# Optimization experiments

Hardware: AMD Instinct MI355X
Metric: run time of the kernel (lower is better)

The kernel has to match this reference:

```python
import jax, jax.numpy as jnp
import numpy as np

D = 64          # d_model
H = 128         # ffn_hidden_dim
N = 10000       # nodes
E = 50000       # edges
NEG_SLOPE = 0.01  # LeakyReLU default


def setup_inputs() -> dict:
    key = jax.random.key(0)
    ks = jax.random.split(key, 10)
    x = jax.random.normal(ks[0], (N, D), dtype=jnp.float32)
    edge_index = jax.random.randint(ks[1], (2, E), 0, N)
    edge_attr = jax.random.normal(ks[2], (E, D), dtype=jnp.float32)
    # MapE2NxN params (stored as [in, out] so forward is x @ W + b)
    w1 = jax.random.normal(ks[3], (D, H), dtype=jnp.float32) / np.sqrt(D)
    b1 = jnp.zeros((H,), dtype=jnp.float32)
    w2 = jax.random.normal(ks[4], (H, D * D), dtype=jnp.float32) / np.sqrt(H)
    b2 = jnp.zeros((D * D,), dtype=jnp.float32)
    # NNConv root weight + bias
    root = jax.random.normal(ks[5], (D, D), dtype=jnp.float32) / np.sqrt(D)
    bias = jnp.zeros((D,), dtype=jnp.float32)
    # LayerNorm affine params
    gamma = jnp.ones((D,), dtype=jnp.float32)
    beta = jnp.zeros((D,), dtype=jnp.float32)
    return {"x": x, "edge_attr": edge_attr, "gamma": gamma, "beta": beta,
            "w1": w1, "b1": b1, "w2": w2, "b2": b2,
            "root": root, "bias": bias, "edge_index": edge_index}


def _layer_norm(h, gamma, beta, eps=1e-5):
    mu = jnp.mean(h, axis=-1, keepdims=True)
    var = jnp.var(h, axis=-1, keepdims=True)
    return (h - mu) * jax.lax.rsqrt(var + eps) * gamma + beta


def _leaky_relu(h):
    return jnp.where(h >= 0, h, NEG_SLOPE * h)


def reference(x, edge_attr, gamma, beta, w1, b1, w2, b2, root, bias, edge_index):
    src, dst = edge_index[0], edge_index[1]
    # DeepGCNLayer block='res+': pre-activation norm -> act -> (dropout p=0) -> conv -> residual
    h = _leaky_relu(_layer_norm(x, gamma, beta))
    # MapE2NxN on edge attributes -> per-edge [D, D] weight matrix
    we = _leaky_relu(edge_attr @ w1 + b1) @ w2 + b2   # [E, D*D]
    we = we.reshape(E, D, D)
    # per-edge matvec with source node features (PyG NNConv message)
    msg = jnp.einsum('ed,edf->ef', h[src], we)        # [E, D]
    # scatter-mean aggregate into destination nodes
    agg = jax.ops.segment_sum(msg, dst, num_segments=N)
    cnt = jax.ops.segment_sum(jnp.ones((E,), dtype=msg.dtype), dst, num_segments=N)
    agg = agg / jnp.maximum(cnt, 1.0)[:, None]
    # root transform + bias, then residual
    out = agg + h @ root + bias
    return x + out
```

## Files before the change

### kernel.cpp

```cpp
#include <hip/hip_runtime.h>

#define NS 10000
#define DD 64
#define HH 128
#define EE 50000
#define SLOPE 0.01f

typedef __attribute__((ext_vector_type(8))) short short8;
typedef __attribute__((ext_vector_type(4))) float f32x4;

static __device__ __forceinline__ unsigned short f2bf(float f) {
  unsigned int u = __float_as_uint(f);
  u += 0x7fff + ((u >> 16) & 1);
  return (unsigned short)(u >> 16);
}

__device__ __forceinline__ float wave_sum64(float v) {
  #pragma unroll
  for (int m = 32; m >= 1; m >>= 1) v += __shfl_xor(v, m, 64);
  return v;
}

__global__ __launch_bounds__(256) void k_tw2z(const float* __restrict__ w2,
    unsigned short* __restrict__ w2t2, float4* __restrict__ zbase, int zn4) {
  __shared__ float tile[64][65];
  int t = threadIdx.x;
  int k = blockIdx.x;
  for (int off = k * 256 + t; off < zn4; off += 128 * 256)
    zbase[off] = make_float4(0.f, 0.f, 0.f, 0.f);
  #pragma unroll
  for (int i = 0; i < 16; ++i) {
    int idx = t + i * 256;
    tile[idx >> 6][idx & 63] = w2[k * (DD * DD) + idx];
  }
  __syncthreads();
  #pragma unroll
  for (int it = 0; it < 2; ++it) {
    int slot = t + it * 256;
    int f = slot >> 3, l8 = slot & 7;
    short8 o;
    #pragma unroll
    for (int j = 0; j < 8; ++j) o[j] = f2bf(tile[l8 * 8 + j][f]);
    *(short8*)(w2t2 + ((size_t)(f * HH + k)) * DD + l8 * 8) = o;
  }
}

__global__ __launch_bounds__(256) void k_prep(const float* __restrict__ x,
    const float* __restrict__ gamma, const float* __restrict__ beta,
    float* __restrict__ h, unsigned short* __restrict__ hbf,
    const float* __restrict__ ea, unsigned short* __restrict__ eabf,
    const float* __restrict__ w1, unsigned short* __restrict__ w1t,
    const float* __restrict__ b2, unsigned short* __restrict__ b2t,
    const int* __restrict__ ei, int* __restrict__ cntsrc,
    int* __restrict__ cntdst) {
  int gid = blockIdx.x * 256 + threadIdx.x;
  if (gid < EE) {
    atomicAdd(&cntsrc[ei[gid]], 1);
    atomicAdd(&cntdst[ei[EE + gid]], 1);
  }
  if (gid < EE * DD / 8) {
    const float4* sp = (const float4*)(ea + (size_t)gid * 8);
    float4 v0 = sp[0], v1 = sp[1];
    short8 o;
    o[0] = f2bf(v0.x); o[1] = f2bf(v0.y); o[2] = f2bf(v0.z); o[3] = f2bf(v0.w);
    o[4] = f2bf(v1.x); o[5] = f2bf(v1.y); o[6] = f2bf(v1.z); o[7] = f2bf(v1.w);
    *(short8*)(eabf + (size_t)gid * 8) = o;
  }
  if (gid < DD * HH) {
    int d = gid & 63, hc = gid >> 6;
    w1t[gid] = f2bf(w1[d * HH + hc]);
  }
  if (gid < DD * DD) {
    int d = gid & 63, f = gid >> 6;
    b2t[gid] = f2bf(b2[d * DD + f]);
  }
  int wid = threadIdx.x >> 6;
  int lane = threadIdx.x & 63;
  int row = blockIdx.x * 4 + wid;
  if (row >= NS) return;
  float v = x[row * DD + lane];
  float s = wave_sum64(v);
  float s2 = wave_sum64(v * v);
  float mu = s * (1.0f / 64.0f);
  float var = s2 * (1.0f / 64.0f) - mu * mu;
  float r = rsqrtf(var + 1e-5f);
  float hn = (v - mu) * r * gamma[lane] + beta[lane];
  float hv = hn >= 0.f ? hn : SLOPE * hn;
  h[row * DD + lane] = hv;
  hbf[row * DD + lane] = f2bf(hv);
}

__global__ __launch_bounds__(1024) void k_scan(const int* __restrict__ cntsrc,
    int* __restrict__ rowptr, int* __restrict__ cursor) {
  __shared__ int ps[1024];
  int t = threadIdx.x;
  const int CH = (NS + 1023) / 1024;
  int base = t * CH;
  int sum = 0;
  for (int i = 0; i < CH; ++i) {
    int idx = base + i;
    if (idx < NS) sum += cntsrc[idx];
  }
  ps[t] = sum;
  __syncthreads();
  for (int off = 1; off < 1024; off <<= 1) {
    int v = (t >= off) ? ps[t - off] : 0;
    __syncthreads();
    ps[t] += v;
    __syncthreads();
  }
  int run = ps[t] - sum;
  for (int i = 0; i < CH; ++i) {
    int idx = base + i;
    if (idx < NS) {
      rowptr[idx] = run;
      cursor[idx] = run;
      run += cntsrc[idx];
    }
  }
  if (t == 1023) rowptr[NS] = run;
}

#define UBLK 782
#define CBLK 157
__global__ __launch_bounds__(256) void k_mid(
    const unsigned short* __restrict__ eabf, const unsigned short* __restrict__ w1t,
    const float* __restrict__ b1, unsigned short* __restrict__ ubf,
    const unsigned short* __restrict__ hbf, const unsigned short* __restrict__ b2t,
    float* __restrict__ cc, const int* __restrict__ ei,
    int* __restrict__ cursor, int* __restrict__ eord) {
  int t = threadIdx.x;
  int bid = blockIdx.x;
  int gid = bid * 256 + t;
  if (gid < EE) {
    int s = ei[gid];
    int pos = atomicAdd(&cursor[s], 1);
    eord[pos] = gid;
  }
  int w = t >> 6, lane = t & 63, lr = lane & 15, lg = lane >> 4;
  if (bid < UBLK) {
    int r0 = bid * 64 + w * 16;
    int ra = r0 + lr; if (ra >= EE) ra = EE - 1;
    short8 a0 = *(const short8*)(eabf + (size_t)ra * DD + lg * 8);
    short8 a1 = *(const short8*)(eabf + (size_t)ra * DD + 32 + lg * 8);
    short8 bb0[8], bb1[8];
    #pragma unroll
    for (int ni = 0; ni < 8; ++ni) {
      const unsigned short* bp = w1t + (ni * 16 + lr) * DD;
      bb0[ni] = *(const short8*)(bp + lg * 8);
      bb1[ni] = *(const short8*)(bp + 32 + lg * 8);
    }
    f32x4 acc[8] = {};
    #pragma unroll
    for (int ni = 0; ni < 8; ++ni) {
      acc[ni] = __builtin_amdgcn_mfma_f32_16x16x32_bf16(a0, bb0[ni], acc[ni], 0, 0, 0);
      acc[ni] = __builtin_amdgcn_mfma_f32_16x16x32_bf16(a1, bb1[ni], acc[ni], 0, 0, 0);
    }
    #pragma unroll
    for (int ni = 0; ni < 8; ++ni) {
      int col = ni * 16 + lr;
      float bb = b1[col];
      #pragma unroll
      for (int reg = 0; reg < 4; ++reg) {
        int gr = r0 + lg * 4 + reg;
        if (gr < EE) {
          float vv = acc[ni][reg] + bb;
          ubf[(size_t)gr * HH + col] = f2bf(vv >= 0.f ? vv : SLOPE * vv);
        }
      }
    }
  } else if (bid < UBLK + CBLK) {
    int row0 = (bid - UBLK) * 64;
    short8 a[4][2];
    #pragma unroll
    for (int mi = 0; mi < 4; ++mi) {
      int ra = row0 + mi * 16 + lr; if (ra >= NS) ra = NS - 1;
      a[mi][0] = *(const short8*)(hbf + (size_t)ra * DD + lg * 8);
      a[mi][1] = *(const short8*)(hbf + (size_t)ra * DD + 32 + lg * 8);
    }
    const unsigned short* bp = b2t + (w * 16 + lr) * DD;
    short8 b0 = *(const short8*)(bp + lg * 8);
    short8 b1v = *(const short8*)(bp + 32 + lg * 8);
    f32x4 acc[4] = {};
    #pragma unroll
    for (int mi = 0; mi < 4; ++mi) {
      acc[mi] = __builtin_amdgcn_mfma_f32_16x16x32_bf16(a[mi][0], b0, acc[mi], 0, 0, 0);
      acc[mi] = __builtin_amdgcn_mfma_f32_16x16x32_bf16(a[mi][1], b1v, acc[mi], 0, 0, 0);
    }
    #pragma unroll
    for (int mi = 0; mi < 4; ++mi)
      #pragma unroll
      for (int reg = 0; reg < 4; ++reg) {
        int gr = row0 + mi * 16 + lg * 4 + reg;
        if (gr < NS) cc[(size_t)gr * DD + w * 16 + lr] = acc[mi][reg];
      }
  }
}

__global__ __launch_bounds__(256) void k_T_mfma(
    const unsigned short* __restrict__ hbf, const unsigned short* __restrict__ w2t2,
    unsigned short* __restrict__ T, int n0, int n1) {
  __shared__ unsigned short As[64][72];
  __shared__ unsigned short Bs[256 * 72];
  int t = threadIdx.x;
  int row0 = n0 + blockIdx.x * 64;
  if (row0 >= n1) return;
  int col0 = blockIdx.y * 256;
  #pragma unroll
  for (int i = 0; i < 2; ++i) {
    int idx = t + i * 256;
    int r = idx >> 3, cc = (idx & 7) * 8;
    int gr = row0 + r;
    short8 v = {};
    if (gr < n1) v = *(const short8*)(hbf + (size_t)gr * DD + cc);
    *(short8*)(&As[r][cc]) = v;
  }
  #pragma unroll
  for (int i = 0; i < 8; ++i) {
    int idx = t + i * 256;
    int cL = idx >> 3, rr = (idx & 7) * 8;
    int gc = col0 + cL;
    short8 v = *(const short8*)(w2t2 + (size_t)gc * DD + rr);
    *(short8*)(&Bs[cL * 72 + rr]) = v;
  }
  __syncthreads();
  int w = t >> 6, lane = t & 63;
  int lr = lane & 15, lg = lane >> 4;
  f32x4 acc[4][4] = {};
  #pragma unroll
  for (int kk = 0; kk < 64; kk += 32) {
    short8 a[4], b[4];
    #pragma unroll
    for (int mi = 0; mi < 4; ++mi)
      a[mi] = *(const short8*)(&As[mi * 16 + lr][kk + lg * 8]);
    #pragma unroll
    for (int ni = 0; ni < 4; ++ni)
      b[ni] = *(const short8*)(&Bs[(w * 64 + ni * 16 + lr) * 72 + kk + lg * 8]);
    #pragma unroll
    for (int mi = 0; mi < 4; ++mi)
      #pragma unroll
      for (int ni = 0; ni < 4; ++ni)
        acc[mi][ni] = __builtin_amdgcn_mfma_f32_16x16x32_bf16(
            a[mi], b[ni], acc[mi][ni], 0, 0, 0);
  }
  __syncthreads();
  #pragma unroll
  for (int mi = 0; mi < 4; ++mi)
    #pragma unroll
    for (int ni = 0; ni < 4; ++ni) {
      int col = w * 64 + ni * 16 + lr;
      #pragma unroll
      for (int reg = 0; reg < 4; ++reg)
        Bs[(mi * 16 + lg * 4 + reg) * 268 + col] = f2bf(acc[mi][ni][reg]);
    }
  __syncthreads();
  #pragma unroll
  for (int i = 0; i < 8; ++i) {
    int idx = t + i * 256;
    int row = idx >> 5, seg = idx & 31;
    int gr = row0 + row;
    if (gr < n1) {
      short8 v = *(const short8*)(&Bs[row * 268 + seg * 8]);
      *(short8*)(T + (size_t)(gr - n0) * (HH * DD) + col0 + seg * 8) = v;
    }
  }
}

__global__ __launch_bounds__(256) void k_msg_wave(
    const unsigned short* __restrict__ ubf, const unsigned short* __restrict__ T,
    const float* __restrict__ cc, const int* __restrict__ ei,
    const int* __restrict__ rowptr, const int* __restrict__ eord,
    float* __restrict__ agg, int n0, int n1) {
  int wid = threadIdx.x >> 6;
  int lane = threadIdx.x & 63;
  int s = n0 + blockIdx.x * 64 + blockIdx.y * 4 + wid;
  if (s >= n1) return;
  int beg = rowptr[s];
  int deg = rowptr[s + 1] - beg;
  if (deg == 0) return;
  int lr = lane & 15, lg = lane >> 4;
  int ev = 0, dv = 0;
  if (lane < 16 && lane < deg) {
    ev = eord[beg + lane];
    dv = ei[EE + ev];
  }
  const unsigned short* tp = T + (size_t)(s - n0) * (HH * DD);
  short8 b[4][4];
  #pragma unroll
  for (int ft = 0; ft < 4; ++ft)
    #pragma unroll
    for (int kk = 0; kk < 4; ++kk)
      b[ft][kk] =
          *(const short8*)(tp + (ft * 16 + lr) * HH + kk * 32 + lg * 8);
  float clv[4];
  #pragma unroll
  for (int ft = 0; ft < 4; ++ft) clv[ft] = cc[(size_t)s * DD + ft * 16 + lr];

  for (int p0 = 0; p0 < deg; p0 += 16) {
    if (p0) {
      ev = 0; dv = 0;
      if (lane < 16 && p0 + lane < deg) {
        ev = eord[beg + p0 + lane];
        dv = ei[EE + ev];
      }
    }
    int el = __shfl(ev, (p0 + lr < deg) ? lr : 0);
    const unsigned short* up = ubf + (size_t)el * HH;
    short8 au[4];
    #pragma unroll
    for (int kk = 0; kk < 4; ++kk)
      au[kk] = *(const short8*)(up + kk * 32 + lg * 8);
    f32x4 acc[4] = {};
    #pragma unroll
    for (int kk = 0; kk < 4; ++kk)
      #pragma unroll
      for (int ft = 0; ft < 4; ++ft)
        acc[ft] = __builtin_amdgcn_mfma_f32_16x16x32_bf16(au[kk], b[ft][kk],
                                                          acc[ft], 0, 0, 0);
    #pragma unroll
    for (int reg = 0; reg < 4; ++reg) {
      int eidx = p0 + lg * 4 + reg;
      int dstn = __shfl(dv, lg * 4 + reg);
      if (eidx < deg) {
        #pragma unroll
        for (int ft = 0; ft < 4; ++ft)
          atomicAdd(&agg[(size_t)dstn * DD + ft * 16 + lr],
                    acc[ft][reg] + clv[ft]);
      }
    }
  }
}

__global__ __launch_bounds__(256) void k_final(const float* __restrict__ x,
    const float* __restrict__ h, const float* __restrict__ root,
    const float* __restrict__ bias, const float* __restrict__ agg,
    const int* __restrict__ cnt, float* __restrict__ out) {
  __shared__ float Bs[DD][DD + 1];
  __shared__ float As[32][DD];
  int t = threadIdx.x;
  #pragma unroll
  for (int i = 0; i < 16; ++i) {
    int idx = t + i * 256;
    Bs[idx >> 6][idx & 63] = root[idx];
  }
  int row0 = blockIdx.x * 32;
  #pragma unroll
  for (int i = 0; i < 8; ++i) {
    int idx = t + i * 256;
    int r = idx >> 6, d = idx & 63;
    int gr = row0 + r;
    As[r][d] = (gr < NS) ? h[gr * DD + d] : 0.f;
  }
  __syncthreads();
  int r = t >> 3;
  int c0 = (t & 7) * 8;
  int gr = row0 + r;
  if (gr >= NS) return;
  float acc[8] = {};
  for (int d = 0; d < DD; ++d) {
    float a = As[r][d];
    #pragma unroll
    for (int j = 0; j < 8; ++j) acc[j] += a * Bs[d][c0 + j];
  }
  float inv = 1.0f / fmaxf((float)cnt[gr], 1.0f);
  #pragma unroll
  for (int j = 0; j < 8; ++j) {
    size_t gi = (size_t)gr * DD + c0 + j;
    out[gi] = x[gi] + agg[gi] * inv + acc[j] + bias[c0 + j];
  }
}

extern "C" void kernel_launch(void* const* d_in, const int* in_sizes, int n_in,
                              void* d_out, int out_size, void* d_ws, size_t ws_size,
                              hipStream_t stream) {
  const float* x     = (const float*)d_in[0];
  const float* ea    = (const float*)d_in[1];
  const float* gamma = (const float*)d_in[2];
  const float* beta  = (const float*)d_in[3];
  const float* w1    = (const float*)d_in[4];
  const float* b1    = (const float*)d_in[5];
  const float* w2    = (const float*)d_in[6];
  const float* b2    = (const float*)d_in[7];
  const float* root  = (const float*)d_in[8];
  const float* bias  = (const float*)d_in[9];
  const int*   ei    = (const int*)d_in[10];
  float* out = (float*)d_out;

  char* p = (char*)d_ws;
  auto carve = [&](size_t bytes) {
    char* q = p;
    p += (bytes + 255) & ~(size_t)255;
    return q;
  };
  float* h             = (float*)carve(sizeof(float) * NS * DD);
  unsigned short* hbf  = (unsigned short*)carve(sizeof(short) * NS * DD);
  float* cc            = (float*)carve(sizeof(float) * NS * DD);
  unsigned short* w2t2 = (unsigned short*)carve(sizeof(short) * HH * DD * DD);
  unsigned short* w1t  = (unsigned short*)carve(sizeof(short) * DD * HH);
  unsigned short* b2t  = (unsigned short*)carve(sizeof(short) * DD * DD);
  unsigned short* eabf = (unsigned short*)carve(sizeof(short) * (size_t)EE * DD);
  unsigned short* ubf  = (unsigned short*)carve(sizeof(short) * (size_t)EE * HH);
  int* rowptr          = (int*)carve(sizeof(int) * (NS + 1));
  int* cursor          = (int*)carve(sizeof(int) * NS);
  int* eord            = (int*)carve(sizeof(int) * EE);
  char* z0 = p;
  float* agg           = (float*)carve(sizeof(float) * NS * DD);
  int* cntdst          = (int*)carve(sizeof(int) * NS);
  int* cntsrc          = (int*)carve(sizeof(int) * NS);
  size_t zlen = (size_t)(p - z0);
  size_t fixed = (size_t)(p - (char*)d_ws);

  size_t freeb = (ws_size > fixed) ? (ws_size - fixed - 256) : 0;
  int rows = (int)(freeb / (sizeof(short) * HH * DD));
  if (rows >= NS) rows = NS;
  else { rows &= ~63; if (rows < 64) rows = 64; }
  unsigned short* Tt = (unsigned short*)carve(sizeof(short) * (size_t)rows * HH * DD);

  k_tw2z<<<dim3(HH), dim3(256), 0, stream>>>(w2, w2t2, (float4*)z0,
                                             (int)(zlen / 16));
  k_prep<<<dim3((NS + 3) / 4), dim3(256), 0, stream>>>(
      x, gamma, beta, h, hbf, ea, eabf, w1, w1t, b2, b2t, ei, cntsrc, cntdst);
  k_scan<<<dim3(1), dim3(1024), 0, stream>>>(cntsrc, rowptr, cursor);
  k_mid<<<dim3(UBLK + CBLK), dim3(256), 0, stream>>>(
      eabf, w1t, b1, ubf, hbf, b2t, cc, ei, cursor, eord);

  for (int n0 = 0; n0 < NS; n0 += rows) {
    int n1 = n0 + rows;
    if (n1 > NS) n1 = NS;
    int nr = n1 - n0;
    int gx = (((nr + 63) / 64) + 7) & ~7;
    k_T_mfma<<<dim3(gx, (HH * DD) / 256), dim3(256), 0, stream>>>(
        hbf, w2t2, Tt, n0, n1);
    k_msg_wave<<<dim3(gx, 16), dim3(256), 0, stream>>>(
        ubf, Tt, cc, ei, rowptr, eord, agg, n0, n1);
  }

  k_final<<<dim3((NS + 31) / 32), dim3(256), 0, stream>>>(x, h, root, bias, agg,
                                                          cntdst, out);
}
```

Measured before the change: 130.2 us.

## Fold weight transpose, scan and edge scatter into neighbouring kernels; narrow T tiles

The w2 transpose moves into extra blocks of k_prep, and the zero-fill becomes a hipMemsetAsync. The single-block prefix scan becomes an extra block of k_mid, and the edge-ordering scatter moves into the first k_T_mfma launch. This cuts the number of serial kernel launches and hides the small serial steps behind larger work. The k_T_mfma column tile is halved from 256 to 128, which uses less LDS and launches more blocks. The tradeoff is that the scan block may lengthen k_mid's tail, and the first T launch takes on extra atomics.

```diff
diff --git a/kernel.cpp b/kernel.cpp
--- a/kernel.cpp
+++ b/kernel.cpp
@@ -21,39 +21,40 @@
   return v;
 }
 
-__global__ __launch_bounds__(256) void k_tw2z(const float* __restrict__ w2,
-    unsigned short* __restrict__ w2t2, float4* __restrict__ zbase, int zn4) {
-  __shared__ float tile[64][65];
-  int t = threadIdx.x;
-  int k = blockIdx.x;
-  for (int off = k * 256 + t; off < zn4; off += 128 * 256)
-    zbase[off] = make_float4(0.f, 0.f, 0.f, 0.f);
-  #pragma unroll
-  for (int i = 0; i < 16; ++i) {
-    int idx = t + i * 256;
-    tile[idx >> 6][idx & 63] = w2[k * (DD * DD) + idx];
-  }
-  __syncthreads();
-  #pragma unroll
-  for (int it = 0; it < 2; ++it) {
-    int slot = t + it * 256;
-    int f = slot >> 3, l8 = slot & 7;
-    short8 o;
-    #pragma unroll
-    for (int j = 0; j < 8; ++j) o[j] = f2bf(tile[l8 * 8 + j][f]);
-    *(short8*)(w2t2 + ((size_t)(f * HH + k)) * DD + l8 * 8) = o;
-  }
-}
-
+#define TBLK 128
 __global__ __launch_bounds__(256) void k_prep(const float* __restrict__ x,
     const float* __restrict__ gamma, const float* __restrict__ beta,
     float* __restrict__ h, unsigned short* __restrict__ hbf,
     const float* __restrict__ ea, unsigned short* __restrict__ eabf,
+    const float* __restrict__ w2, unsigned short* __restrict__ w2t2,
     const float* __restrict__ w1, unsigned short* __restrict__ w1t,
     const float* __restrict__ b2, unsigned short* __restrict__ b2t,
     const int* __restrict__ ei, int* __restrict__ cntsrc,
     int* __restrict__ cntdst) {
-  int gid = blockIdx.x * 256 + threadIdx.x;
+  __shared__ float tile[64][65];
+  int t = threadIdx.x;
+  int bid = blockIdx.x;
+  if (bid < TBLK) {
+    int k = bid;
+    #pragma unroll
+    for (int i = 0; i < 16; ++i) {
+      int idx = t + i * 256;
+      tile[idx >> 6][idx & 63] = w2[k * (DD * DD) + idx];
+    }
+    __syncthreads();
+    #pragma unroll
+    for (int it = 0; it < 2; ++it) {
+      int slot = t + it * 256;
+      int f = slot >> 3, l8 = slot & 7;
+      short8 o;
+      #pragma unroll
+      for (int j = 0; j < 8; ++j) o[j] = f2bf(tile[l8 * 8 + j][f]);
+      *(short8*)(w2t2 + ((size_t)(f * HH + k)) * DD + l8 * 8) = o;
+    }
+    return;
+  }
+  int pbid = bid - TBLK;
+  int gid = pbid * 256 + t;
   if (gid < EE) {
     atomicAdd(&cntsrc[ei[gid]], 1);
     atomicAdd(&cntdst[ei[EE + gid]], 1);
@@ -74,9 +75,9 @@
     int d = gid & 63, f = gid >> 6;
     b2t[gid] = f2bf(b2[d * DD + f]);
   }
-  int wid = threadIdx.x >> 6;
-  int lane = threadIdx.x & 63;
-  int row = blockIdx.x * 4 + wid;
+  int wid = t >> 6;
+  int lane = t & 63;
+  int row = pbid * 4 + wid;
   if (row >= NS) return;
   float v = x[row * DD + lane];
   float s = wave_sum64(v);
@@ -90,53 +91,16 @@
   hbf[row * DD + lane] = f2bf(hv);
 }
 
-__global__ __launch_bounds__(1024) void k_scan(const int* __restrict__ cntsrc,
-    int* __restrict__ rowptr, int* __restrict__ cursor) {
-  __shared__ int ps[1024];
-  int t = threadIdx.x;
-  const int CH = (NS + 1023) / 1024;
-  int base = t * CH;
-  int sum = 0;
-  for (int i = 0; i < CH; ++i) {
-    int idx = base + i;
-    if (idx < NS) sum += cntsrc[idx];
-  }
-  ps[t] = sum;
-  __syncthreads();
-  for (int off = 1; off < 1024; off <<= 1) {
-    int v = (t >= off) ? ps[t - off] : 0;
-    __syncthreads();
-    ps[t] += v;
-    __syncthreads();
-  }
-  int run = ps[t] - sum;
-  for (int i = 0; i < CH; ++i) {
-    int idx = base + i;
-    if (idx < NS) {
-      rowptr[idx] = run;
-      cursor[idx] = run;
-      run += cntsrc[idx];
-    }
-  }
-  if (t == 1023) rowptr[NS] = run;
-}
-
 #define UBLK 782
 #define CBLK 157
 __global__ __launch_bounds__(256) void k_mid(
     const unsigned short* __restrict__ eabf, const unsigned short* __restrict__ w1t,
     const float* __restrict__ b1, unsigned short* __restrict__ ubf,
     const unsigned short* __restrict__ hbf, const unsigned short* __restrict__ b2t,
-    float* __restrict__ cc, const int* __restrict__ ei,
-    int* __restrict__ cursor, int* __restrict__ eord) {
+    float* __restrict__ cc, const int* __restrict__ cntsrc,
+    int* __restrict__ rowptr, int* __restrict__ cursor) {
   int t = threadIdx.x;
   int bid = blockIdx.x;
-  int gid = bid * 256 + t;
-  if (gid < EE) {
-    int s = ei[gid];
-    int pos = atomicAdd(&cursor[s], 1);
-    eord[pos] = gid;
-  }
   int w = t >> 6, lane = t & 63, lr = lane & 15, lg = lane >> 4;
   if (bid < UBLK) {
     int r0 = bid * 64 + w * 16;
@@ -194,18 +158,55 @@
         int gr = row0 + mi * 16 + lg * 4 + reg;
         if (gr < NS) cc[(size_t)gr * DD + w * 16 + lr] = acc[mi][reg];
       }
+  } else {
+    __shared__ int ps[256];
+    const int CH = (NS + 255) / 256;
+    int base = t * CH;
+    int sum = 0;
+    for (int i = 0; i < CH; ++i) {
+      int idx = base + i;
+      if (idx < NS) sum += cntsrc[idx];
+    }
+    ps[t] = sum;
+    __syncthreads();
+    for (int off = 1; off < 256; off <<= 1) {
+      int v = (t >= off) ? ps[t - off] : 0;
+      __syncthreads();
+      ps[t] += v;
+      __syncthreads();
+    }
+    int run = ps[t] - sum;
+    for (int i = 0; i < CH; ++i) {
+      int idx = base + i;
+      if (idx < NS) {
+        rowptr[idx] = run;
+        cursor[idx] = run;
+        run += cntsrc[idx];
+      }
+    }
+    if (t == 255) rowptr[NS] = run;
   }
 }
 
 __global__ __launch_bounds__(256) void k_T_mfma(
     const unsigned short* __restrict__ hbf, const unsigned short* __restrict__ w2t2,
-    unsigned short* __restrict__ T, int n0, int n1) {
+    unsigned short* __restrict__ T, int n0, int n1, int gx,
+    const int* __restrict__ ei, int* __restrict__ cursor,
+    int* __restrict__ eord, int doScatter) {
   __shared__ unsigned short As[64][72];
-  __shared__ unsigned short Bs[256 * 72];
+  __shared__ unsigned short Bs[128 * 72];
   int t = threadIdx.x;
+  if (doScatter) {
+    int gid = (blockIdx.y * gx + blockIdx.x) * 256 + t;
+    if (gid < EE) {
+      int s = ei[gid];
+      int pos = atomicAdd(&cursor[s], 1);
+      eord[pos] = gid;
+    }
+  }
   int row0 = n0 + blockIdx.x * 64;
   if (row0 >= n1) return;
-  int col0 = blockIdx.y * 256;
+  int col0 = blockIdx.y * 128;
   #pragma unroll
   for (int i = 0; i < 2; ++i) {
     int idx = t + i * 256;
@@ -216,7 +217,7 @@
     *(short8*)(&As[r][cc]) = v;
   }
   #pragma unroll
-  for (int i = 0; i < 8; ++i) {
+  for (int i = 0; i < 4; ++i) {
     int idx = t + i * 256;
     int cL = idx >> 3, rr = (idx & 7) * 8;
     int gc = col0 + cL;
@@ -226,20 +227,20 @@
   __syncthreads();
   int w = t >> 6, lane = t & 63;
   int lr = lane & 15, lg = lane >> 4;
-  f32x4 acc[4][4] = {};
+  f32x4 acc[4][2] = {};
   #pragma unroll
   for (int kk = 0; kk < 64; kk += 32) {
-    short8 a[4], b[4];
+    short8 a[4], b[2];
     #pragma unroll
     for (int mi = 0; mi < 4; ++mi)
       a[mi] = *(const short8*)(&As[mi * 16 + lr][kk + lg * 8]);
     #pragma unroll
-    for (int ni = 0; ni < 4; ++ni)
-      b[ni] = *(const short8*)(&Bs[(w * 64 + ni * 16 + lr) * 72 + kk + lg * 8]);
+    for (int ni = 0; ni < 2; ++ni)
+      b[ni] = *(const short8*)(&Bs[(w * 32 + ni * 16 + lr) * 72 + kk + lg * 8]);
     #pragma unroll
     for (int mi = 0; mi < 4; ++mi)
       #pragma unroll
-      for (int ni = 0; ni < 4; ++ni)
+      for (int ni = 0; ni < 2; ++ni)
         acc[mi][ni] = __builtin_amdgcn_mfma_f32_16x16x32_bf16(
             a[mi], b[ni], acc[mi][ni], 0, 0, 0);
   }
@@ -247,20 +248,20 @@
   #pragma unroll
   for (int mi = 0; mi < 4; ++mi)
     #pragma unroll
-    for (int ni = 0; ni < 4; ++ni) {
-      int col = w * 64 + ni * 16 + lr;
+    for (int ni = 0; ni < 2; ++ni) {
+      int col = w * 32 + ni * 16 + lr;
       #pragma unroll
       for (int reg = 0; reg < 4; ++reg)
-        Bs[(mi * 16 + lg * 4 + reg) * 268 + col] = f2bf(acc[mi][ni][reg]);
+        Bs[(mi * 16 + lg * 4 + reg) * 132 + col] = f2bf(acc[mi][ni][reg]);
     }
   __syncthreads();
   #pragma unroll
-  for (int i = 0; i < 8; ++i) {
+  for (int i = 0; i < 4; ++i) {
     int idx = t + i * 256;
-    int row = idx >> 5, seg = idx & 31;
+    int row = idx >> 4, seg = idx & 15;
     int gr = row0 + row;
     if (gr < n1) {
-      short8 v = *(const short8*)(&Bs[row * 268 + seg * 8]);
+      short8 v = *(const short8*)(&Bs[row * 132 + seg * 8]);
       *(short8*)(T + (size_t)(gr - n0) * (HH * DD) + col0 + seg * 8) = v;
     }
   }
@@ -416,21 +417,20 @@
   else { rows &= ~63; if (rows < 64) rows = 64; }
   unsigned short* Tt = (unsigned short*)carve(sizeof(short) * (size_t)rows * HH * DD);
 
-  k_tw2z<<<dim3(HH), dim3(256), 0, stream>>>(w2, w2t2, (float4*)z0,
-                                             (int)(zlen / 16));
-  k_prep<<<dim3((NS + 3) / 4), dim3(256), 0, stream>>>(
-      x, gamma, beta, h, hbf, ea, eabf, w1, w1t, b2, b2t, ei, cntsrc, cntdst);
-  k_scan<<<dim3(1), dim3(1024), 0, stream>>>(cntsrc, rowptr, cursor);
-  k_mid<<<dim3(UBLK + CBLK), dim3(256), 0, stream>>>(
-      eabf, w1t, b1, ubf, hbf, b2t, cc, ei, cursor, eord);
+  hipMemsetAsync(z0, 0, zlen, stream);
+  k_prep<<<dim3(TBLK + (NS + 3) / 4), dim3(256), 0, stream>>>(
+      x, gamma, beta, h, hbf, ea, eabf, w2, w2t2, w1, w1t, b2, b2t,
+      ei, cntsrc, cntdst);
+  k_mid<<<dim3(UBLK + CBLK + 1), dim3(256), 0, stream>>>(
+      eabf, w1t, b1, ubf, hbf, b2t, cc, cntsrc, rowptr, cursor);
 
   for (int n0 = 0; n0 < NS; n0 += rows) {
     int n1 = n0 + rows;
     if (n1 > NS) n1 = NS;
     int nr = n1 - n0;
     int gx = (((nr + 63) / 64) + 7) & ~7;
-    k_T_mfma<<<dim3(gx, (HH * DD) / 256), dim3(256), 0, stream>>>(
-        hbf, w2t2, Tt, n0, n1);
+    k_T_mfma<<<dim3(gx, (HH * DD) / 128), dim3(256), 0, stream>>>(
+        hbf, w2t2, Tt, n0, n1, gx, ei, cursor, eord, n0 == 0 ? 1 : 0);
     k_msg_wave<<<dim3(gx, 16), dim3(256), 0, stream>>>(
         ubf, Tt, cc, ei, rowptr, eord, agg, n0, n1);
   }
```

Result: slower. 136.1 us (+4.5%).
